# Kernel tuning notes

Hardware: AMD Instinct MI355X
Metric: run time of the kernel (lower is better)

Reference implementation:

```python
import jax, jax.numpy as jnp
import numpy as np

B, S, F_IN, F_OUT, K = 4, 4096, 64, 64, 32


def setup_inputs() -> dict:
    key = jax.random.key(0)
    k1, k2, k3 = jax.random.split(key, 3)
    X = jax.random.normal(k1, (B, S, F_IN), dtype=jnp.float32)
    M = jax.random.normal(k2, (B, S, K), dtype=jnp.float32)
    # xavier_uniform for weight: bound = sqrt(6/(fan_in+fan_out))
    bound = float(np.sqrt(6.0 / (F_IN + F_OUT)))
    weight = jax.random.uniform(k3, (F_IN, F_OUT), dtype=jnp.float32,
                                minval=-bound, maxval=bound)
    bias = jnp.zeros((F_OUT,), dtype=jnp.float32)
    return {"X": X, "M": M, "weight": weight, "bias": bias}


def reference(X, M, weight, bias):
    # similarity = softmax(relu(M M^T), axis=-1)  -> [B, S, S]
    sim_raw = jnp.einsum('bsk,btk->bst', M, M)
    sim = jax.nn.softmax(jax.nn.relu(sim_raw), axis=-1)
    # X W  -> [B, S, F_OUT]
    Xw = jnp.einsum('bsf,fo->bso', X, weight)
    # mode='add': (I + A) Xw = Xw + A @ Xw  (identity matmul folded)
    Z = Xw + jnp.einsum('bst,bto->bso', sim, Xw)
    Z = Z + bias
    # dropout is identity at inference (eval mode)
    return Z
```

## Files before the change

### kernel.cpp

```cpp
#include <hip/hip_runtime.h>
#include <cstdint>

#define BATCH  4
#define SLEN   4096
#define FDIM   64
#define KDIM   32
#define KSPLIT 8
#define CHUNK  (SLEN / KSPLIT)
#define NSTEP  (CHUNK / 32)

#define MSCALE 1.2011224087864498f

typedef __attribute__((ext_vector_type(8))) short bf16x8;
typedef __attribute__((ext_vector_type(4))) short bf16x4;
typedef __attribute__((ext_vector_type(4))) float f32x4;

#if __has_builtin(__builtin_amdgcn_exp2f)
#define EXP2(x) __builtin_amdgcn_exp2f(x)
#else
#define EXP2(x) exp2f(x)
#endif

static __device__ __forceinline__ short f2bf(float f) {
    union { float f; unsigned u; } v; v.f = f;
    unsigned r = v.u + 0x7fffu + ((v.u >> 16) & 1u);
    return (short)(r >> 16);
}
static __device__ __forceinline__ float bf2f(short s) {
    union { unsigned u; float f; } v;
    v.u = ((unsigned)(unsigned short)s) << 16;
    return v.f;
}
static __device__ __forceinline__ unsigned pack2bf(float a, float b) {
    union { float f; unsigned u; } x, y; x.f = a; y.f = b;
    unsigned ra = x.u + 0x7fffu + ((x.u >> 16) & 1u);
    unsigned rb = y.u + 0x7fffu + ((y.u >> 16) & 1u);
    return __builtin_amdgcn_perm(rb, ra, 0x07060302u);
}

__global__ __launch_bounds__(256) void prep(const float4* __restrict__ M4,
                                            ushort4* __restrict__ H4,
                                            ushort4* __restrict__ L4,
                                            const float4* __restrict__ X4,
                                            const float4* __restrict__ W4,
                                            float4* __restrict__ V4,
                                            short* __restrict__ Vt) {
    const int tid = threadIdx.x;
    const int blk = blockIdx.y * gridDim.x + blockIdx.x;
    if (blk < (BATCH * SLEN * KDIM) / (4 * 256)) {
        int i = blk * 256 + tid;
        float4 m = M4[i];
        float mx = m.x * MSCALE, my = m.y * MSCALE;
        float mz = m.z * MSCALE, mw = m.w * MSCALE;
        ushort4 h, l;
        h.x = (unsigned short)f2bf(mx); l.x = (unsigned short)f2bf(mx - bf2f((short)h.x));
        h.y = (unsigned short)f2bf(my); l.y = (unsigned short)f2bf(my - bf2f((short)h.y));
        h.z = (unsigned short)f2bf(mz); l.z = (unsigned short)f2bf(mz - bf2f((short)h.z));
        h.w = (unsigned short)f2bf(mw); l.w = (unsigned short)f2bf(mw - bf2f((short)h.w));
        H4[i] = h; L4[i] = l;
    }
    __shared__ float t[16][68];
    const int b  = blockIdx.y;
    const int s0 = blockIdx.x * 16;
    const int r  = tid >> 4;
    const int o4 = tid & 15;
    const float4* __restrict__ xr = X4 + ((size_t)b * SLEN + s0 + r) * (FDIM / 4);
    float4 acc = make_float4(0.f, 0.f, 0.f, 0.f);
#pragma unroll
    for (int f4 = 0; f4 < FDIM / 4; ++f4) {
        float4 x  = xr[f4];
        float4 w0 = W4[(f4 * 4 + 0) * 16 + o4];
        float4 w1 = W4[(f4 * 4 + 1) * 16 + o4];
        float4 w2 = W4[(f4 * 4 + 2) * 16 + o4];
        float4 w3 = W4[(f4 * 4 + 3) * 16 + o4];
        acc.x = fmaf(x.x, w0.x, fmaf(x.y, w1.x, fmaf(x.z, w2.x, fmaf(x.w, w3.x, acc.x))));
        acc.y = fmaf(x.x, w0.y, fmaf(x.y, w1.y, fmaf(x.z, w2.y, fmaf(x.w, w3.y, acc.y))));
        acc.z = fmaf(x.x, w0.z, fmaf(x.y, w1.z, fmaf(x.z, w2.z, fmaf(x.w, w3.z, acc.z))));
        acc.w = fmaf(x.x, w0.w, fmaf(x.y, w1.w, fmaf(x.z, w2.w, fmaf(x.w, w3.w, acc.w))));
    }
    V4[((size_t)b * SLEN + s0 + r) * 16 + o4] = acc;
    t[r][o4 * 4 + 0] = acc.x;
    t[r][o4 * 4 + 1] = acc.y;
    t[r][o4 * 4 + 2] = acc.z;
    t[r][o4 * 4 + 3] = acc.w;
    __syncthreads();
    const int c  = tid & 15;
    const int f0 = tid >> 4;
#pragma unroll
    for (int i2 = 0; i2 < 4; ++i2) {
        int f = f0 + i2 * 16;
        Vt[((size_t)b * FDIM + f) * SLEN + s0 + c] = f2bf(t[c][f]);
    }
}

__global__ __launch_bounds__(256, 3) void attn_mfma(const short* __restrict__ Mhi,
                                                    const short* __restrict__ Mlo,
                                                    const short* __restrict__ Vt,
                                                    float* __restrict__ accP,
                                                    float* __restrict__ lP) {
    const int bid  = blockIdx.x;
    const int slab = (bid & 7) + 8 * (bid >> 8);
    const int qblk = (bid >> 3) & 31;
    const int b    = slab >> 3;
    const int ks   = slab & 7;

    const int tid  = threadIdx.x;
    const int wave = tid >> 6;
    const int lane = tid & 63;
    const int col  = lane & 15;
    const int quad = lane >> 4;
    const int qbase = qblk * 128 + wave * 32;
    const int k0    = ks * CHUNK;

    const short* __restrict__ Mbh = Mhi + (size_t)b * SLEN * KDIM;
    const short* __restrict__ Mbl = Mlo + (size_t)b * SLEN * KDIM;
    const short* __restrict__ Vb  = Vt  + (size_t)b * FDIM * SLEN;

    __shared__ short khi[2][32 * 40];
    __shared__ short klo[2][32 * 40];
    __shared__ short vsh[2][64 * 40];

    bf16x8 Qh[2], Ql[2];
#pragma unroll
    for (int tq = 0; tq < 2; ++tq) {
        int qo = (qbase + tq * 16 + col) * KDIM + quad * 8;
        Qh[tq] = *(const bf16x8*)(Mbh + qo);
        Ql[tq] = *(const bf16x8*)(Mbl + qo);
    }

    f32x4 accf[2][4];
#pragma unroll
    for (int tq = 0; tq < 2; ++tq)
#pragma unroll
        for (int fg = 0; fg < 4; ++fg) accf[tq][fg] = (f32x4){0.f, 0.f, 0.f, 0.f};
    float lacc[2] = {0.f, 0.f};

    const int krow  = (tid & 127) >> 2;
    const int kpart = tid & 3;
    const int vrow  = tid >> 2;
    const short* __restrict__ Msrc = (tid < 128) ? Mbh : Mbl;
    const int koff  = krow * 40 + kpart * 8;
    const int voff  = vrow * 40 + kpart * 8;
    const int kgoff = krow * KDIM + kpart * 8;

    bf16x8 kstg = *(const bf16x8*)(Msrc + (size_t)k0 * KDIM + kgoff);
    bf16x8 vstg = *(const bf16x8*)(Vb + (size_t)vrow * SLEN + k0 + kpart * 8);

#pragma unroll 1
    for (int step = 0; step < NSTEP; ++step) {
        const int cur = step & 1;
        short* __restrict__ kdst = (tid < 128) ? khi[cur] : klo[cur];
        *(bf16x8*)(kdst + koff)     = kstg;
        *(bf16x8*)(vsh[cur] + voff) = vstg;
        if (step + 1 < NSTEP) {
            int kt = k0 + (step + 1) * 32;
            kstg = *(const bf16x8*)(Msrc + (size_t)kt * KDIM + kgoff);
            vstg = *(const bf16x8*)(Vb + (size_t)vrow * SLEN + kt + kpart * 8);
        }
        asm volatile("s_waitcnt lgkmcnt(0)" ::: "memory");
        __builtin_amdgcn_s_barrier();
        __builtin_amdgcn_sched_barrier(0);

        const short* __restrict__ kh = khi[cur];
        const short* __restrict__ kl = klo[cur];
        const short* __restrict__ vv = vsh[cur];

        bf16x8 Kh0 = *(const bf16x8*)(kh + col * 40 + quad * 8);
        bf16x8 Kh1 = *(const bf16x8*)(kh + (16 + col) * 40 + quad * 8);
        bf16x8 Kl0 = *(const bf16x8*)(kl + col * 40 + quad * 8);
        bf16x8 Kl1 = *(const bf16x8*)(kl + (16 + col) * 40 + quad * 8);

        bf16x8 Vv[4];
#pragma unroll
        for (int fg = 0; fg < 4; ++fg) {
            const short* vp = vv + (fg * 16 + col) * 40 + quad * 4;
            bf16x4 vlo = *(const bf16x4*)(vp);
            bf16x4 vhi = *(const bf16x4*)(vp + 16);
            Vv[fg] = __builtin_shufflevector(vlo, vhi, 0, 1, 2, 3, 4, 5, 6, 7);
        }

        __builtin_amdgcn_s_setprio(1);
#pragma unroll
        for (int tq = 0; tq < 2; ++tq) {
            f32x4 z = (f32x4){0.f, 0.f, 0.f, 0.f};
            f32x4 c0 = __builtin_amdgcn_mfma_f32_16x16x32_bf16(Kh0, Ql[tq], z, 0, 0, 0);
            f32x4 c1 = __builtin_amdgcn_mfma_f32_16x16x32_bf16(Kh1, Ql[tq], z, 0, 0, 0);
            c0 = __builtin_amdgcn_mfma_f32_16x16x32_bf16(Kl0, Qh[tq], c0, 0, 0, 0);
            c1 = __builtin_amdgcn_mfma_f32_16x16x32_bf16(Kl1, Qh[tq], c1, 0, 0, 0);
            c0 = __builtin_amdgcn_mfma_f32_16x16x32_bf16(Kh0, Qh[tq], c0, 0, 0, 0);
            c1 = __builtin_amdgcn_mfma_f32_16x16x32_bf16(Kh1, Qh[tq], c1, 0, 0, 0);

            float e00 = EXP2(fmaxf(c0[0], 0.f));
            float e01 = EXP2(fmaxf(c0[1], 0.f));
            float e02 = EXP2(fmaxf(c0[2], 0.f));
            float e03 = EXP2(fmaxf(c0[3], 0.f));
            float e10 = EXP2(fmaxf(c1[0], 0.f));
            float e11 = EXP2(fmaxf(c1[1], 0.f));
            float e12 = EXP2(fmaxf(c1[2], 0.f));
            float e13 = EXP2(fmaxf(c1[3], 0.f));
            lacc[tq] += ((e00 + e01) + (e02 + e03)) + ((e10 + e11) + (e12 + e13));

            union { unsigned u[4]; bf16x8 v; } pa;
            pa.u[0] = pack2bf(e00, e01);
            pa.u[1] = pack2bf(e02, e03);
            pa.u[2] = pack2bf(e10, e11);
            pa.u[3] = pack2bf(e12, e13);

#pragma unroll
            for (int fg = 0; fg < 4; ++fg)
                accf[tq][fg] = __builtin_amdgcn_mfma_f32_16x16x32_bf16(
                    pa.v, Vv[fg], accf[tq][fg], 0, 0, 0);
        }
        __builtin_amdgcn_s_setprio(0);
    }

#pragma unroll
    for (int tq = 0; tq < 2; ++tq) {
#pragma unroll
        for (int j = 0; j < 4; ++j) {
            int q = qbase + tq * 16 + quad * 4 + j;
            size_t base = ((size_t)b * SLEN + q) * KSPLIT + ks;
            float* __restrict__ op = accP + base * FDIM;
#pragma unroll
            for (int fg = 0; fg < 4; ++fg)
                op[fg * 16 + col] = accf[tq][fg][j];
        }
        float lv = lacc[tq];
        lv += __shfl_xor(lv, 16);
        lv += __shfl_xor(lv, 32);
        if (quad == 0) {
            int q = qbase + tq * 16 + col;
            lP[((size_t)b * SLEN + q) * KSPLIT + ks] = lv;
        }
    }
}

__global__ __launch_bounds__(256) void combine_kernel(const float4* __restrict__ V4,
                                                      const float4* __restrict__ accP4,
                                                      const float4* __restrict__ lP4,
                                                      const float4* __restrict__ bias4,
                                                      float4* __restrict__ out4) {
    int i  = blockIdx.x * 256 + threadIdx.x;
    int o4 = i & 15;
    int row = i >> 4;
    float nx = 0.f, ny = 0.f, nz = 0.f, nw = 0.f;
#pragma unroll
    for (int k = 0; k < KSPLIT; ++k) {
        float4 a = accP4[((size_t)row * KSPLIT + k) * 16 + o4];
        nx += a.x; ny += a.y; nz += a.z; nw += a.w;
    }
    float4 l0 = lP4[(size_t)row * 2 + 0];
    float4 l1 = lP4[(size_t)row * 2 + 1];
    float den = ((l0.x + l0.y) + (l0.z + l0.w)) + ((l1.x + l1.y) + (l1.z + l1.w));
    float r = 1.f / den;
    float4 v = V4[i];
    float4 bb = bias4[o4];
    float4 o;
    o.x = v.x + nx * r + bb.x;
    o.y = v.y + ny * r + bb.y;
    o.z = v.z + nz * r + bb.z;
    o.w = v.w + nw * r + bb.w;
    out4[i] = o;
}

extern "C" void kernel_launch(void* const* d_in, const int* in_sizes, int n_in,
                              void* d_out, int out_size, void* d_ws, size_t ws_size,
                              hipStream_t stream) {
    const float* X    = (const float*)d_in[0];
    const float* M    = (const float*)d_in[1];
    const float* W    = (const float*)d_in[2];
    const float* bias = (const float*)d_in[3];
    float* out = (float*)d_out;

    const size_t vElems = (size_t)BATCH * SLEN * FDIM;
    const size_t mElems = (size_t)BATCH * SLEN * KDIM;
    const size_t rows   = (size_t)BATCH * SLEN;

    float* Vf   = (float*)d_ws;
    float* accP = Vf + vElems;
    float* lP   = accP + vElems * KSPLIT;
    short* Mhi  = (short*)(lP + rows * KSPLIT);
    short* Mlo  = Mhi + mElems;
    short* Vt   = Mlo + mElems;

    prep<<<dim3(SLEN / 16, BATCH), 256, 0, stream>>>(
        (const float4*)M, (ushort4*)Mhi, (ushort4*)Mlo,
        (const float4*)X, (const float4*)W, (float4*)Vf, Vt);

    attn_mfma<<<dim3((SLEN / 128) * BATCH * KSPLIT), 256, 0, stream>>>(
        Mhi, Mlo, Vt, accP, lP);

    combine_kernel<<<(int)(vElems / 1024), 256, 0, stream>>>(
        (const float4*)Vf, (const float4*)accP, (const float4*)lP,
        (const float4*)bias, (float4*)out);
}
```

Measured before the change: 113.1 us.

## Halve key split, double key tile per step, use hardware bf16 pack

The attention kernel now splits the key dimension 4 ways instead of 8 and processes 64 keys per pipeline step instead of 32. This halves the number of barriers and partial-sum writes and gives each step more MFMA work per staged tile. The shared V tile gets a padded stride of 76 to avoid bank conflicts. The software bf16 rounding-and-pack sequence is replaced by the v_cvt_pk_bf16_f32 instruction. In exchange the grid has half as many blocks, the occupancy hint drops from 3 to 2 blocks per SIMD group, and register and LDS use per block rise, which may reduce latency hiding on a 256-CU part.

```diff
diff --git a/kernel.cpp b/kernel.cpp
--- a/kernel.cpp
+++ b/kernel.cpp
@@ -5,9 +5,10 @@
 #define SLEN   4096
 #define FDIM   64
 #define KDIM   32
-#define KSPLIT 8
+#define KSPLIT 4
 #define CHUNK  (SLEN / KSPLIT)
-#define NSTEP  (CHUNK / 32)
+#define NSTEP  (CHUNK / 64)
+#define VSTRIDE 76
 
 #define MSCALE 1.2011224087864498f
 
@@ -31,11 +32,10 @@
     v.u = ((unsigned)(unsigned short)s) << 16;
     return v.f;
 }
-static __device__ __forceinline__ unsigned pack2bf(float a, float b) {
-    union { float f; unsigned u; } x, y; x.f = a; y.f = b;
-    unsigned ra = x.u + 0x7fffu + ((x.u >> 16) & 1u);
-    unsigned rb = y.u + 0x7fffu + ((y.u >> 16) & 1u);
-    return __builtin_amdgcn_perm(rb, ra, 0x07060302u);
+static __device__ __forceinline__ unsigned cvt_pk_bf16(float a, float b) {
+    unsigned r;
+    asm("v_cvt_pk_bf16_f32 %0, %1, %2" : "=v"(r) : "v"(a), "v"(b));
+    return r;
 }
 
 __global__ __launch_bounds__(256) void prep(const float4* __restrict__ M4,
@@ -93,7 +93,7 @@
     }
 }
 
-__global__ __launch_bounds__(256, 3) void attn_mfma(const short* __restrict__ Mhi,
+__global__ __launch_bounds__(256, 2) void attn_mfma(const short* __restrict__ Mhi,
                                                     const short* __restrict__ Mlo,
                                                     const short* __restrict__ Vt,
                                                     float* __restrict__ accP,
@@ -101,8 +101,8 @@
     const int bid  = blockIdx.x;
     const int slab = (bid & 7) + 8 * (bid >> 8);
     const int qblk = (bid >> 3) & 31;
-    const int b    = slab >> 3;
-    const int ks   = slab & 7;
+    const int b    = slab >> 2;
+    const int ks   = slab & 3;
 
     const int tid  = threadIdx.x;
     const int wave = tid >> 6;
@@ -116,9 +116,9 @@
     const short* __restrict__ Mbl = Mlo + (size_t)b * SLEN * KDIM;
     const short* __restrict__ Vb  = Vt  + (size_t)b * FDIM * SLEN;
 
-    __shared__ short khi[2][32 * 40];
-    __shared__ short klo[2][32 * 40];
-    __shared__ short vsh[2][64 * 40];
+    __shared__ short khi[2][64 * 40];
+    __shared__ short klo[2][64 * 40];
+    __shared__ short vsh[2][64 * VSTRIDE];
 
     bf16x8 Qh[2], Ql[2];
 #pragma unroll
@@ -135,27 +135,37 @@
         for (int fg = 0; fg < 4; ++fg) accf[tq][fg] = (f32x4){0.f, 0.f, 0.f, 0.f};
     float lacc[2] = {0.f, 0.f};
 
-    const int krow  = (tid & 127) >> 2;
-    const int kpart = tid & 3;
-    const int vrow  = tid >> 2;
+    const int krow = (tid & 127) >> 1;
+    const int kp   = tid & 1;
+    const int vrow = tid >> 2;
+    const int vp   = tid & 3;
     const short* __restrict__ Msrc = (tid < 128) ? Mbh : Mbl;
-    const int koff  = krow * 40 + kpart * 8;
-    const int voff  = vrow * 40 + kpart * 8;
-    const int kgoff = krow * KDIM + kpart * 8;
-
-    bf16x8 kstg = *(const bf16x8*)(Msrc + (size_t)k0 * KDIM + kgoff);
-    bf16x8 vstg = *(const bf16x8*)(Vb + (size_t)vrow * SLEN + k0 + kpart * 8);
+    const int kg0 = krow * KDIM + (kp * 2 + 0) * 8;
+    const int kg1 = krow * KDIM + (kp * 2 + 1) * 8;
+    const int kl0 = krow * 40 + (kp * 2 + 0) * 8;
+    const int kl1 = krow * 40 + (kp * 2 + 1) * 8;
+    const int vl0 = vrow * VSTRIDE + (vp + 0) * 8;
+    const int vl1 = vrow * VSTRIDE + (vp + 4) * 8;
+
+    bf16x8 ksA = *(const bf16x8*)(Msrc + (size_t)k0 * KDIM + kg0);
+    bf16x8 ksB = *(const bf16x8*)(Msrc + (size_t)k0 * KDIM + kg1);
+    bf16x8 vsA = *(const bf16x8*)(Vb + (size_t)vrow * SLEN + k0 + (vp + 0) * 8);
+    bf16x8 vsB = *(const bf16x8*)(Vb + (size_t)vrow * SLEN + k0 + (vp + 4) * 8);
 
 #pragma unroll 1
     for (int step = 0; step < NSTEP; ++step) {
         const int cur = step & 1;
         short* __restrict__ kdst = (tid < 128) ? khi[cur] : klo[cur];
-        *(bf16x8*)(kdst + koff)     = kstg;
-        *(bf16x8*)(vsh[cur] + voff) = vstg;
+        *(bf16x8*)(kdst + kl0)     = ksA;
+        *(bf16x8*)(kdst + kl1)     = ksB;
+        *(bf16x8*)(vsh[cur] + vl0) = vsA;
+        *(bf16x8*)(vsh[cur] + vl1) = vsB;
         if (step + 1 < NSTEP) {
-            int kt = k0 + (step + 1) * 32;
-            kstg = *(const bf16x8*)(Msrc + (size_t)kt * KDIM + kgoff);
-            vstg = *(const bf16x8*)(Vb + (size_t)vrow * SLEN + kt + kpart * 8);
+            int kt = k0 + (step + 1) * 64;
+            ksA = *(const bf16x8*)(Msrc + (size_t)kt * KDIM + kg0);
+            ksB = *(const bf16x8*)(Msrc + (size_t)kt * KDIM + kg1);
+            vsA = *(const bf16x8*)(Vb + (size_t)vrow * SLEN + kt + (vp + 0) * 8);
+            vsB = *(const bf16x8*)(Vb + (size_t)vrow * SLEN + kt + (vp + 4) * 8);
         }
         asm volatile("s_waitcnt lgkmcnt(0)" ::: "memory");
         __builtin_amdgcn_s_barrier();
@@ -165,51 +175,62 @@
         const short* __restrict__ kl = klo[cur];
         const short* __restrict__ vv = vsh[cur];
 
-        bf16x8 Kh0 = *(const bf16x8*)(kh + col * 40 + quad * 8);
-        bf16x8 Kh1 = *(const bf16x8*)(kh + (16 + col) * 40 + quad * 8);
-        bf16x8 Kl0 = *(const bf16x8*)(kl + col * 40 + quad * 8);
-        bf16x8 Kl1 = *(const bf16x8*)(kl + (16 + col) * 40 + quad * 8);
-
-        bf16x8 Vv[4];
-#pragma unroll
-        for (int fg = 0; fg < 4; ++fg) {
-            const short* vp = vv + (fg * 16 + col) * 40 + quad * 4;
-            bf16x4 vlo = *(const bf16x4*)(vp);
-            bf16x4 vhi = *(const bf16x4*)(vp + 16);
-            Vv[fg] = __builtin_shufflevector(vlo, vhi, 0, 1, 2, 3, 4, 5, 6, 7);
-        }
+        bf16x8 Kh[4], Kl[4];
+#pragma unroll
+        for (int t = 0; t < 4; ++t) {
+            Kh[t] = *(const bf16x8*)(kh + (t * 16 + col) * 40 + quad * 8);
+            Kl[t] = *(const bf16x8*)(kl + (t * 16 + col) * 40 + quad * 8);
+        }
+        bf16x8 Vg[4][2];
+#pragma unroll
+        for (int fg = 0; fg < 4; ++fg)
+#pragma unroll
+            for (int g = 0; g < 2; ++g) {
+                const short* vp_ = vv + (fg * 16 + col) * VSTRIDE + g * 32 + quad * 4;
+                bf16x4 vlo = *(const bf16x4*)(vp_);
+                bf16x4 vhi = *(const bf16x4*)(vp_ + 16);
+                Vg[fg][g] = __builtin_shufflevector(vlo, vhi, 0, 1, 2, 3, 4, 5, 6, 7);
+            }
 
         __builtin_amdgcn_s_setprio(1);
 #pragma unroll
         for (int tq = 0; tq < 2; ++tq) {
-            f32x4 z = (f32x4){0.f, 0.f, 0.f, 0.f};
-            f32x4 c0 = __builtin_amdgcn_mfma_f32_16x16x32_bf16(Kh0, Ql[tq], z, 0, 0, 0);
-            f32x4 c1 = __builtin_amdgcn_mfma_f32_16x16x32_bf16(Kh1, Ql[tq], z, 0, 0, 0);
-            c0 = __builtin_amdgcn_mfma_f32_16x16x32_bf16(Kl0, Qh[tq], c0, 0, 0, 0);
-            c1 = __builtin_amdgcn_mfma_f32_16x16x32_bf16(Kl1, Qh[tq], c1, 0, 0, 0);
-            c0 = __builtin_amdgcn_mfma_f32_16x16x32_bf16(Kh0, Qh[tq], c0, 0, 0, 0);
-            c1 = __builtin_amdgcn_mfma_f32_16x16x32_bf16(Kh1, Qh[tq], c1, 0, 0, 0);
-
-            float e00 = EXP2(fmaxf(c0[0], 0.f));
-            float e01 = EXP2(fmaxf(c0[1], 0.f));
-            float e02 = EXP2(fmaxf(c0[2], 0.f));
-            float e03 = EXP2(fmaxf(c0[3], 0.f));
-            float e10 = EXP2(fmaxf(c1[0], 0.f));
-            float e11 = EXP2(fmaxf(c1[1], 0.f));
-            float e12 = EXP2(fmaxf(c1[2], 0.f));
-            float e13 = EXP2(fmaxf(c1[3], 0.f));
-            lacc[tq] += ((e00 + e01) + (e02 + e03)) + ((e10 + e11) + (e12 + e13));
-
-            union { unsigned u[4]; bf16x8 v; } pa;
-            pa.u[0] = pack2bf(e00, e01);
-            pa.u[1] = pack2bf(e02, e03);
-            pa.u[2] = pack2bf(e10, e11);
-            pa.u[3] = pack2bf(e12, e13);
-
-#pragma unroll
-            for (int fg = 0; fg < 4; ++fg)
+            f32x4 c[4];
+#pragma unroll
+            for (int t = 0; t < 4; ++t) {
+                f32x4 z = (f32x4){0.f, 0.f, 0.f, 0.f};
+                c[t] = __builtin_amdgcn_mfma_f32_16x16x32_bf16(Kh[t], Ql[tq], z, 0, 0, 0);
+                c[t] = __builtin_amdgcn_mfma_f32_16x16x32_bf16(Kl[t], Qh[tq], c[t], 0, 0, 0);
+                c[t] = __builtin_amdgcn_mfma_f32_16x16x32_bf16(Kh[t], Qh[tq], c[t], 0, 0, 0);
+            }
+            float e[16];
+#pragma unroll
+            for (int t = 0; t < 4; ++t) {
+                e[t * 4 + 0] = EXP2(fmaxf(c[t][0], 0.f));
+                e[t * 4 + 1] = EXP2(fmaxf(c[t][1], 0.f));
+                e[t * 4 + 2] = EXP2(fmaxf(c[t][2], 0.f));
+                e[t * 4 + 3] = EXP2(fmaxf(c[t][3], 0.f));
+            }
+            lacc[tq] += (((e[0] + e[1]) + (e[2] + e[3])) + ((e[4] + e[5]) + (e[6] + e[7])))
+                      + (((e[8] + e[9]) + (e[10] + e[11])) + ((e[12] + e[13]) + (e[14] + e[15])));
+
+            union { unsigned u[4]; bf16x8 v; } pa0, pa1;
+            pa0.u[0] = cvt_pk_bf16(e[0],  e[1]);
+            pa0.u[1] = cvt_pk_bf16(e[2],  e[3]);
+            pa0.u[2] = cvt_pk_bf16(e[4],  e[5]);
+            pa0.u[3] = cvt_pk_bf16(e[6],  e[7]);
+            pa1.u[0] = cvt_pk_bf16(e[8],  e[9]);
+            pa1.u[1] = cvt_pk_bf16(e[10], e[11]);
+            pa1.u[2] = cvt_pk_bf16(e[12], e[13]);
+            pa1.u[3] = cvt_pk_bf16(e[14], e[15]);
+
+#pragma unroll
+            for (int fg = 0; fg < 4; ++fg) {
                 accf[tq][fg] = __builtin_amdgcn_mfma_f32_16x16x32_bf16(
-                    pa.v, Vv[fg], accf[tq][fg], 0, 0, 0);
+                    pa0.v, Vg[fg][0], accf[tq][fg], 0, 0, 0);
+                accf[tq][fg] = __builtin_amdgcn_mfma_f32_16x16x32_bf16(
+                    pa1.v, Vg[fg][1], accf[tq][fg], 0, 0, 0);
+            }
         }
         __builtin_amdgcn_s_setprio(0);
     }
@@ -249,9 +270,8 @@
         float4 a = accP4[((size_t)row * KSPLIT + k) * 16 + o4];
         nx += a.x; ny += a.y; nz += a.z; nw += a.w;
     }
-    float4 l0 = lP4[(size_t)row * 2 + 0];
-    float4 l1 = lP4[(size_t)row * 2 + 1];
-    float den = ((l0.x + l0.y) + (l0.z + l0.w)) + ((l1.x + l1.y) + (l1.z + l1.w));
+    float4 l = lP4[row];
+    float den = (l.x + l.y) + (l.z + l.w);
     float r = 1.f / den;
     float4 v = V4[i];
     float4 bb = bias4[o4];
```

Result: faster. 109.0 us (median of 2 runs) (-3.6%).
